# Performance work log

Measured on AMD Instinct MI355X. Metric: run time of the kernel, lower is better.

The kernel has to match this reference:

```python
import jax, jax.numpy as jnp
import numpy as np

N = 96                       # max_num_nodes == input_dim
LATENT = 256
OUT_DIM = N * (N + 1) // 2   # 4656
MPM_ITERS = 50


def setup_inputs() -> dict:
    key = jax.random.key(0)
    ks = jax.random.split(key, 8)
    s = 0.05
    return {
        "input_features": jax.random.normal(ks[0], (1, N, N), jnp.float32),
        "adj": jax.random.uniform(ks[1], (1, N, N), jnp.float32),
        "eps": jax.random.normal(ks[2], (1, LATENT), jnp.float32),
        "We11": jax.random.normal(ks[3], (N * N, LATENT), jnp.float32) * s,
        "be11": jnp.zeros((LATENT,), jnp.float32),
        "We12": jax.random.normal(ks[4], (N * N, LATENT), jnp.float32) * s,
        "be12": jnp.zeros((LATENT,), jnp.float32),
        "Wd1": jax.random.normal(ks[5], (LATENT, LATENT), jnp.float32) * s,
        "bd1": jnp.zeros((LATENT,), jnp.float32),
        "Wd2": jax.random.normal(ks[6], (LATENT, OUT_DIM), jnp.float32) * s,
        "bd2": jnp.zeros((OUT_DIM,), jnp.float32),
    }


def _bce(inp, tgt):
    # torch F.binary_cross_entropy(input=inp, target=tgt) with log clamp -100
    li = jnp.clip(jnp.log(inp), -100.0)
    l1 = jnp.clip(jnp.log1p(-inp), -100.0)
    return -jnp.mean(tgt * li + (1.0 - tgt) * l1)


def reference(input_features, adj, eps, We11, be11, We12, be12, Wd1, bd1, Wd2, bd2):
    # ---- MLP_VAE_plain ----
    h = input_features.reshape(-1, N * N)              # [1, N*N]
    z_mu = h @ We11 + be11
    z_ls = h @ We12 + be12
    z = eps * jnp.exp(0.5 * z_ls) + z_mu
    y = jax.nn.relu(z @ Wd1 + bd1) @ Wd2 + bd2         # [1, OUT_DIM]
    out = jax.nn.sigmoid(y)

    # ---- recover recon adjacency from triu vector (detached in original) ----
    iu, ju = jnp.triu_indices(N)
    up = jnp.zeros((N, N), jnp.float32).at[iu, ju].set(out[0])
    adj_rec = up + up.T - jnp.diag(jnp.diag(up))

    adj0 = adj[0]
    feat = jnp.sum(adj0, axis=1)                       # degree features
    feat_r = jnp.sum(adj_rec, axis=1)

    # ---- edge similarity tensor S[i,j,a,b] (vectorized O(N^4)) ----
    d = jnp.diag(adj0)
    dr = jnp.diag(adj_rec)
    A = adj0 * d[:, None] * d[None, :]                 # adj[i,j]*adj[i,i]*adj[j,j]
    B = adj_rec * dr[:, None] * dr[None, :]
    off = 1.0 - jnp.eye(N, dtype=jnp.float32)
    S = (A * off)[:, :, None, None] * (B * off)[None, None, :, :]  # i!=j, a!=b
    sim = 1.0 / (jnp.abs(feat[:, None] - feat_r[None, :]) + 1.0)   # deg_feature_similarity
    Sd = d[:, None] * dr[None, :] * sim                # S[i,i,a,a]
    r = jnp.arange(N)
    S = S.at[r[:, None], r[:, None], r[None, :], r[None, :]].set(Sd)

    # ---- max-pool matching (mpm), 50 iterations ----
    x0 = jnp.full((N, N), 1.0 / N, jnp.float32)

    def step(x, _):
        pooled = jnp.max(S * x[None, :, None, :], axis=3)          # [i,j,a]
        x_new = x * Sd + jnp.einsum('ija,ij->ia', pooled, off)     # sum over j != i
        return x_new / jnp.linalg.norm(x_new), None

    assignment, _ = jax.lax.scan(step, x0, None, length=MPM_ITERS)
    # (original then calls scipy Hungarian and only prints; result is unused in loss)

    # ---- loss ----
    adj_vec = adj0[iu, ju]                             # detached in original
    recon_loss = _bce(adj_vec, out[0])
    kl = -0.5 * jnp.sum(1.0 + z_ls - z_mu ** 2 - jnp.exp(z_ls)) / (N * N)
    loss = recon_loss + kl
    return loss, assignment
```

## Files before the change

### kernel.cpp

```cpp
#include <hip/hip_runtime.h>
#include <math.h>

typedef unsigned long long ull;

#define N      96
#define NN     9216
#define LAT    256
#define ODIM   4656
#define CH     128
#define RPC    72
#define ITERS  50
#define CB     12
#define CT     768
#define CPB    8

#define SGNMASK2 0x8000000080000000ULL
#define ABSMASK2 0x7FFFFFFF7FFFFFFFULL

#define WS_PART  0
#define WS_OUTS  65536
#define WS_KL    70192
#define WS_BCE   70193
#define WS_NSLOT 70208
#define WS_XBUF  70592

__device__ __forceinline__ int tri(int i, int j) {
    return i * N - i * (i - 1) / 2 + (j - i);
}

__device__ __forceinline__ int tri_row(int o) {
    int i = (int)floorf((193.0f - sqrtf((float)(37249 - 8 * o))) * 0.5f);
    i = max(0, min(95, i));
    while ((i + 1) * N - (i + 1) * i / 2 <= o) ++i;
    while (i * N - i * (i - 1) / 2 > o) --i;
    return i;
}

__global__ __launch_bounds__(256) void kA_gemv(const float* __restrict__ h,
                                               const float* __restrict__ W1,
                                               const float* __restrict__ W2,
                                               float* __restrict__ ws) {
    __shared__ float hs[RPC];
    int t = threadIdx.x, c = blockIdx.x;
    if (c == 0) {
        if (t < 2) ws[WS_KL + t] = 0.f;
        if (t < CB * 16) {
            ws[WS_NSLOT + t]           = 0.0f;
            ws[WS_NSLOT + CB * 16 + t] = -0.0f;
        }
    }
    for (int z = c * 256 + t; z < NN; z += CH * 256) {
        ws[WS_XBUF + z]      = 0.0f;
        ws[WS_XBUF + NN + z] = -0.0f;
    }
    int k0 = c * RPC;
    if (t < RPC) hs[t] = h[k0 + t];
    __syncthreads();
    float a1 = 0.f, a2 = 0.f;
    #pragma unroll 4
    for (int kk = 0; kk < RPC; ++kk) {
        float hv = hs[kk];
        a1 = fmaf(hv, W1[(k0 + kk) * LAT + t], a1);
        a2 = fmaf(hv, W2[(k0 + kk) * LAT + t], a2);
    }
    ws[WS_PART + c * LAT + t]        = a1;
    ws[WS_PART + (CH + c) * LAT + t] = a2;
}

__global__ __launch_bounds__(256) void kB_dec(const float* __restrict__ eps,
                                              const float* __restrict__ be11,
                                              const float* __restrict__ be12,
                                              const float* __restrict__ Wd1,
                                              const float* __restrict__ bd1,
                                              const float* __restrict__ Wd2,
                                              const float* __restrict__ bd2,
                                              const float* __restrict__ adj,
                                              float* __restrict__ ws) {
    __shared__ float zi[LAT];
    __shared__ float hid[LAT];
    __shared__ float red[256];
    int t = threadIdx.x;
    const float* p = ws + WS_PART;
    float mu = 0.f, ls = 0.f;
    #pragma unroll 8
    for (int c = 0; c < CH; ++c) {
        mu += p[c * LAT + t];
        ls += p[(CH + c) * LAT + t];
    }
    mu += be11[t];
    ls += be12[t];
    zi[t] = eps[t] * expf(0.5f * ls) + mu;
    red[t] = 1.0f + ls - mu * mu - expf(ls);
    __syncthreads();
    for (int s = 128; s > 0; s >>= 1) {
        if (t < s) red[t] += red[t + s];
        __syncthreads();
    }
    if (blockIdx.x == 0 && t == 0) ws[WS_KL] = -0.5f * red[0] / 9216.0f;
    __syncthreads();
    float acc = 0.f;
    #pragma unroll 8
    for (int k = 0; k < LAT; ++k) acc = fmaf(zi[k], Wd1[k * LAT + t], acc);
    hid[t] = fmaxf(acc + bd1[t], 0.f);
    __syncthreads();
    int o = blockIdx.x * 256 + t;
    float term = 0.f;
    if (o < ODIM) {
        float a2 = 0.f;
        #pragma unroll 8
        for (int k = 0; k < LAT; ++k) a2 = fmaf(hid[k], Wd2[k * ODIM + o], a2);
        float y = a2 + bd2[o];
        float s = 1.0f / (1.0f + expf(-y));
        ws[WS_OUTS + o] = s;
        int i = tri_row(o);
        int j = i + (o - (i * N - i * (i - 1) / 2));
        float inp = adj[i * N + j];
        float li = fmaxf(logf(inp), -100.0f);
        float l1 = fmaxf(log1pf(-inp), -100.0f);
        term = s * li + (1.0f - s) * l1;
    }
    red[t] = term;
    __syncthreads();
    for (int s = 128; s > 0; s >>= 1) {
        if (t < s) red[t] += red[t + s];
        __syncthreads();
    }
    if (t == 0) atomicAdd(ws + WS_BCE, red[0]);
}

__global__ __launch_bounds__(CT, 3) void kC_mpm(const float* __restrict__ adj,
                                                float* __restrict__ ws,
                                                float* __restrict__ out) {
    __shared__ float xnT[N][97];
    __shared__ float Brow[CPB][N];
    __shared__ float Scol[CPB][N];
    __shared__ float Mv[CPB][N];
    __shared__ float ds[N], drs[N], ft[N];
    __shared__ float ftr_sh[CPB];
    __shared__ float wred[CT / 64];
    __shared__ float s_inv;

    int t = threadIdx.x, bid = blockIdx.x;
    int jj = t % N, al = t / N;
    int a  = bid * CPB + al;

    const float* outs = ws + WS_OUTS;
    float* xbuf  = ws + WS_XBUF;
    float* nslot = ws + WS_NSLOT;

    if (t < N) {
        ds[t]  = adj[t * N + t];
        drs[t] = outs[tri(t, t)];
        const float4* ar = (const float4*)(adj + t * N);
        float s1 = 0.f;
        #pragma unroll
        for (int q = 0; q < N / 4; ++q) {
            float4 v = ar[q];
            s1 += v.x + v.y + v.z + v.w;
        }
        ft[t] = s1;
    }
    __syncthreads();
    {
        int lo = min(a, jj), hi = max(a, jj);
        Mv[al][jj] = outs[tri(lo, hi)];
    }
    __syncthreads();
    if (t < CPB) {
        float s2 = 0.f;
        for (int b = 0; b < N; ++b) s2 += Mv[t][b];
        ftr_sh[t] = s2;
    }
    __syncthreads();
    Brow[al][jj] = (jj == a) ? 0.f : (Mv[al][jj] * drs[a]) * drs[jj];
    Scol[al][jj] = (ds[jj] * drs[a]) * (1.0f / (fabsf(ft[jj] - ftr_sh[al]) + 1.0f));

    float arow[N];
    {
        const float* arp = adj + jj * N;
        float di = ds[jj];
        #pragma unroll
        for (int j = 0; j < N; ++j)
            arow[j] = (j == jj) ? 0.f : (arp[j] * di) * ds[j];
    }
    __syncthreads();

    float acc = 0.f;
    for (int s = 0; s < ITERS; ++s) {
        if (s == 0) {
            const float v0 = (float)(1.0 / 96.0);
            for (int f = t; f < NN; f += CT) xnT[f / N][f % N] = v0;
            if (t == 0) s_inv = 1.0f;
        } else {
            const ull want = ((s >> 1) & 1) ? SGNMASK2 : 0ULL;
            const ull* src = (const ull*)(xbuf + (s & 1) * NN);
            ull v[6];
            bool ok = false;
            while (!ok) {
                ok = true;
                #pragma unroll
                for (int k = 0; k < 6; ++k)
                    v[k] = __hip_atomic_load(&src[k * CT + t], __ATOMIC_RELAXED,
                                             __HIP_MEMORY_SCOPE_AGENT);
                #pragma unroll
                for (int k = 0; k < 6; ++k)
                    ok &= ((v[k] & SGNMASK2) == want);
                if (!ok) __builtin_amdgcn_s_sleep(1);
            }
            #pragma unroll
            for (int k = 0; k < 6; ++k) {
                ull w = v[k] & ABSMASK2;
                int e = (k * CT + t) * 2;
                int ac = e / N, i = e % N;
                xnT[ac][i]     = __uint_as_float((unsigned)w);
                xnT[ac][i + 1] = __uint_as_float((unsigned)(w >> 32));
            }
            if (t < 64) {
                const unsigned esn = (unsigned)((s >> 1) & 1);
                float pv = 0.f;
                bool done = (t >= CB);
                const unsigned* np = (const unsigned*)(nslot + (s & 1) * CB * 16);
                while (!__all(done)) {
                    if (!done) {
                        unsigned u = __hip_atomic_load(&np[t * 16], __ATOMIC_RELAXED,
                                                       __HIP_MEMORY_SCOPE_AGENT);
                        if ((u >> 31) == esn) { pv = __uint_as_float(u & 0x7FFFFFFFu); done = true; }
                    }
                    __builtin_amdgcn_s_sleep(1);
                }
                #pragma unroll
                for (int off = 8; off > 0; off >>= 1) pv += __shfl_xor(pv, off, 16);
                if (t == 0) s_inv = 1.0f / sqrtf(pv);
            }
        }
        __syncthreads();

        float m = 0.f;
        #pragma unroll
        for (int bq = 0; bq < N / 4; ++bq) {
            m = fmaxf(m, Brow[al][bq * 4 + 0] * xnT[bq * 4 + 0][jj]);
            m = fmaxf(m, Brow[al][bq * 4 + 1] * xnT[bq * 4 + 1][jj]);
            m = fmaxf(m, Brow[al][bq * 4 + 2] * xnT[bq * 4 + 2][jj]);
            m = fmaxf(m, Brow[al][bq * 4 + 3] * xnT[bq * 4 + 3][jj]);
        }
        Mv[al][jj] = m;
        __syncthreads();

        float r = xnT[a][jj] * Scol[al][jj];
        #pragma unroll
        for (int q = 0; q < N / 4; ++q) {
            float4 mv = *(const float4*)&Mv[al][q * 4];
            r = fmaf(arow[q * 4 + 0], mv.x, r);
            r = fmaf(arow[q * 4 + 1], mv.y, r);
            r = fmaf(arow[q * 4 + 2], mv.z, r);
            r = fmaf(arow[q * 4 + 3], mv.w, r);
        }
        acc = r * s_inv;

        const unsigned tag1 = (unsigned)(((s + 1) >> 1) & 1);
        float nx = __shfl_down(acc, 1);
        if (s < ITERS - 1 && (t & 1) == 0) {
            ull pv = (ull)__float_as_uint(acc) | ((ull)__float_as_uint(nx) << 32);
            if (tag1) pv |= SGNMASK2;
            __hip_atomic_store((ull*)(xbuf + ((s + 1) & 1) * NN) + ((a * N + jj) >> 1),
                               pv, __ATOMIC_RELAXED, __HIP_MEMORY_SCOPE_AGENT);
        }

        float ssq = acc * acc;
        #pragma unroll
        for (int off = 32; off > 0; off >>= 1) ssq += __shfl_xor(ssq, off);
        if ((t & 63) == 0) wred[t >> 6] = ssq;
        __syncthreads();
        if (t == 0) {
            float sum = 0.f;
            #pragma unroll
            for (int w = 0; w < CT / 64; ++w) sum += wred[w];
            unsigned u = __float_as_uint(sum) | (tag1 << 31);
            __hip_atomic_store((unsigned*)(nslot + ((s + 1) & 1) * CB * 16 + bid * 16),
                               u, __ATOMIC_RELAXED, __HIP_MEMORY_SCOPE_AGENT);
        }
    }

    if (t < 64) {
        const unsigned esf = (unsigned)((ITERS >> 1) & 1);
        float pv = 0.f;
        bool done = (t >= CB);
        const unsigned* np = (const unsigned*)(nslot + (ITERS & 1) * CB * 16);
        while (!__all(done)) {
            if (!done) {
                unsigned u = __hip_atomic_load(&np[t * 16], __ATOMIC_RELAXED,
                                               __HIP_MEMORY_SCOPE_AGENT);
                if ((u >> 31) == esf) { pv = __uint_as_float(u & 0x7FFFFFFFu); done = true; }
            }
            __builtin_amdgcn_s_sleep(1);
        }
        #pragma unroll
        for (int off = 8; off > 0; off >>= 1) pv += __shfl_xor(pv, off, 16);
        if (t == 0) s_inv = 1.0f / sqrtf(pv);
    }
    __syncthreads();
    out[1 + jj * N + a] = acc * s_inv;
    if (bid == 0 && t == 0)
        out[0] = -(ws[WS_BCE] / 4656.0f) + ws[WS_KL];
}

extern "C" void kernel_launch(void* const* d_in, const int* in_sizes, int n_in,
                              void* d_out, int out_size, void* d_ws, size_t ws_size,
                              hipStream_t stream) {
    const float* inf  = (const float*)d_in[0];
    const float* adj  = (const float*)d_in[1];
    const float* eps  = (const float*)d_in[2];
    const float* We11 = (const float*)d_in[3];
    const float* be11 = (const float*)d_in[4];
    const float* We12 = (const float*)d_in[5];
    const float* be12 = (const float*)d_in[6];
    const float* Wd1  = (const float*)d_in[7];
    const float* bd1  = (const float*)d_in[8];
    const float* Wd2  = (const float*)d_in[9];
    const float* bd2  = (const float*)d_in[10];
    float* ws  = (float*)d_ws;
    float* out = (float*)d_out;

    kA_gemv<<<CH, 256, 0, stream>>>(inf, We11, We12, ws);
    kB_dec <<<19, 256, 0, stream>>>(eps, be11, be12, Wd1, bd1, Wd2, bd2, adj, ws);
    kC_mpm <<<CB, CT, 0, stream>>>(adj, ws, out);
}
```

Measured before the change: 365.9 us.

## Compute norm locally from gathered x instead of cross-block norm slots

Drops the separate per-block sum-of-squares slots and the polling on them. Each block now recomputes the global norm from the full x vector it already gathers every iteration, reducing it across its waves in shared memory. This removes one inter-block handshake and a block barrier per iteration. In exchange, every block does redundant squared-sum work, and the final iteration must also publish and re-gather the whole x vector to normalise the output.

```diff
diff --git a/kernel.cpp b/kernel.cpp
--- a/kernel.cpp
+++ b/kernel.cpp
@@ -21,7 +21,6 @@
 #define WS_OUTS  65536
 #define WS_KL    70192
 #define WS_BCE   70193
-#define WS_NSLOT 70208
 #define WS_XBUF  70592
 
 __device__ __forceinline__ int tri(int i, int j) {
@@ -42,13 +41,7 @@
                                                float* __restrict__ ws) {
     __shared__ float hs[RPC];
     int t = threadIdx.x, c = blockIdx.x;
-    if (c == 0) {
-        if (t < 2) ws[WS_KL + t] = 0.f;
-        if (t < CB * 16) {
-            ws[WS_NSLOT + t]           = 0.0f;
-            ws[WS_NSLOT + CB * 16 + t] = -0.0f;
-        }
-    }
+    if (c == 0 && t < 2) ws[WS_KL + t] = 0.f;
     for (int z = c * 256 + t; z < NN; z += CH * 256) {
         ws[WS_XBUF + z]      = 0.0f;
         ws[WS_XBUF + NN + z] = -0.0f;
@@ -138,15 +131,14 @@
     __shared__ float ds[N], drs[N], ft[N];
     __shared__ float ftr_sh[CPB];
     __shared__ float wred[CT / 64];
-    __shared__ float s_inv;
 
     int t = threadIdx.x, bid = blockIdx.x;
+    int wv = t >> 6;
     int jj = t % N, al = t / N;
     int a  = bid * CPB + al;
 
     const float* outs = ws + WS_OUTS;
     float* xbuf  = ws + WS_XBUF;
-    float* nslot = ws + WS_NSLOT;
 
     if (t < N) {
         ds[t]  = adj[t * N + t];
@@ -190,7 +182,6 @@
         if (s == 0) {
             const float v0 = (float)(1.0 / 96.0);
             for (int f = t; f < NN; f += CT) xnT[f / N][f % N] = v0;
-            if (t == 0) s_inv = 1.0f;
         } else {
             const ull want = ((s >> 1) & 1) ? SGNMASK2 : 0ULL;
             const ull* src = (const ull*)(xbuf + (s & 1) * NN);
@@ -207,31 +198,21 @@
                     ok &= ((v[k] & SGNMASK2) == want);
                 if (!ok) __builtin_amdgcn_s_sleep(1);
             }
+            float tssq = 0.f;
             #pragma unroll
             for (int k = 0; k < 6; ++k) {
                 ull w = v[k] & ABSMASK2;
                 int e = (k * CT + t) * 2;
                 int ac = e / N, i = e % N;
-                xnT[ac][i]     = __uint_as_float((unsigned)w);
-                xnT[ac][i + 1] = __uint_as_float((unsigned)(w >> 32));
+                float f0 = __uint_as_float((unsigned)w);
+                float f1 = __uint_as_float((unsigned)(w >> 32));
+                xnT[ac][i]     = f0;
+                xnT[ac][i + 1] = f1;
+                tssq = fmaf(f0, f0, fmaf(f1, f1, tssq));
             }
-            if (t < 64) {
-                const unsigned esn = (unsigned)((s >> 1) & 1);
-                float pv = 0.f;
-                bool done = (t >= CB);
-                const unsigned* np = (const unsigned*)(nslot + (s & 1) * CB * 16);
-                while (!__all(done)) {
-                    if (!done) {
-                        unsigned u = __hip_atomic_load(&np[t * 16], __ATOMIC_RELAXED,
-                                                       __HIP_MEMORY_SCOPE_AGENT);
-                        if ((u >> 31) == esn) { pv = __uint_as_float(u & 0x7FFFFFFFu); done = true; }
-                    }
-                    __builtin_amdgcn_s_sleep(1);
-                }
-                #pragma unroll
-                for (int off = 8; off > 0; off >>= 1) pv += __shfl_xor(pv, off, 16);
-                if (t == 0) s_inv = 1.0f / sqrtf(pv);
-            }
+            #pragma unroll
+            for (int off = 32; off > 0; off >>= 1) tssq += __shfl_xor(tssq, off);
+            if ((t & 63) == 0) wred[wv] = tssq;
         }
         __syncthreads();
 
@@ -245,6 +226,16 @@
         }
         Mv[al][jj] = m;
         __syncthreads();
+
+        float s_inv;
+        if (s == 0) {
+            s_inv = 1.0f;
+        } else {
+            float sum = 0.f;
+            #pragma unroll
+            for (int w = 0; w < CT / 64; ++w) sum += wred[w];
+            s_inv = 1.0f / sqrtf(sum);
+        }
 
         float r = xnT[a][jj] * Scol[al][jj];
         #pragma unroll
@@ -259,49 +250,51 @@
 
         const unsigned tag1 = (unsigned)(((s + 1) >> 1) & 1);
         float nx = __shfl_down(acc, 1);
-        if (s < ITERS - 1 && (t & 1) == 0) {
+        if ((t & 1) == 0) {
             ull pv = (ull)__float_as_uint(acc) | ((ull)__float_as_uint(nx) << 32);
             if (tag1) pv |= SGNMASK2;
             __hip_atomic_store((ull*)(xbuf + ((s + 1) & 1) * NN) + ((a * N + jj) >> 1),
                                pv, __ATOMIC_RELAXED, __HIP_MEMORY_SCOPE_AGENT);
         }
-
-        float ssq = acc * acc;
-        #pragma unroll
-        for (int off = 32; off > 0; off >>= 1) ssq += __shfl_xor(ssq, off);
-        if ((t & 63) == 0) wred[t >> 6] = ssq;
-        __syncthreads();
-        if (t == 0) {
-            float sum = 0.f;
-            #pragma unroll
-            for (int w = 0; w < CT / 64; ++w) sum += wred[w];
-            unsigned u = __float_as_uint(sum) | (tag1 << 31);
-            __hip_atomic_store((unsigned*)(nslot + ((s + 1) & 1) * CB * 16 + bid * 16),
-                               u, __ATOMIC_RELAXED, __HIP_MEMORY_SCOPE_AGENT);
-        }
-    }
-
-    if (t < 64) {
-        const unsigned esf = (unsigned)((ITERS >> 1) & 1);
-        float pv = 0.f;
-        bool done = (t >= CB);
-        const unsigned* np = (const unsigned*)(nslot + (ITERS & 1) * CB * 16);
-        while (!__all(done)) {
-            if (!done) {
-                unsigned u = __hip_atomic_load(&np[t * 16], __ATOMIC_RELAXED,
-                                               __HIP_MEMORY_SCOPE_AGENT);
-                if ((u >> 31) == esf) { pv = __uint_as_float(u & 0x7FFFFFFFu); done = true; }
-            }
-            __builtin_amdgcn_s_sleep(1);
-        }
-        #pragma unroll
-        for (int off = 8; off > 0; off >>= 1) pv += __shfl_xor(pv, off, 16);
-        if (t == 0) s_inv = 1.0f / sqrtf(pv);
-    }
-    __syncthreads();
-    out[1 + jj * N + a] = acc * s_inv;
-    if (bid == 0 && t == 0)
-        out[0] = -(ws[WS_BCE] / 4656.0f) + ws[WS_KL];
+        __syncthreads();
+    }
+
+    {
+        const ull want = ((ITERS >> 1) & 1) ? SGNMASK2 : 0ULL;
+        const ull* src = (const ull*)(xbuf + (ITERS & 1) * NN);
+        ull v[6];
+        bool ok = false;
+        while (!ok) {
+            ok = true;
+            #pragma unroll
+            for (int k = 0; k < 6; ++k)
+                v[k] = __hip_atomic_load(&src[k * CT + t], __ATOMIC_RELAXED,
+                                         __HIP_MEMORY_SCOPE_AGENT);
+            #pragma unroll
+            for (int k = 0; k < 6; ++k)
+                ok &= ((v[k] & SGNMASK2) == want);
+            if (!ok) __builtin_amdgcn_s_sleep(1);
+        }
+        float tssq = 0.f;
+        #pragma unroll
+        for (int k = 0; k < 6; ++k) {
+            ull w = v[k] & ABSMASK2;
+            float f0 = __uint_as_float((unsigned)w);
+            float f1 = __uint_as_float((unsigned)(w >> 32));
+            tssq = fmaf(f0, f0, fmaf(f1, f1, tssq));
+        }
+        #pragma unroll
+        for (int off = 32; off > 0; off >>= 1) tssq += __shfl_xor(tssq, off);
+        if ((t & 63) == 0) wred[wv] = tssq;
+        __syncthreads();
+        float sum = 0.f;
+        #pragma unroll
+        for (int w = 0; w < CT / 64; ++w) sum += wred[w];
+        float s_invf = 1.0f / sqrtf(sum);
+        out[1 + jj * N + a] = acc * s_invf;
+        if (bid == 0 && t == 0)
+            out[0] = -(ws[WS_BCE] / 4656.0f) + ws[WS_KL];
+    }
 }
 
 extern "C" void kernel_launch(void* const* d_in, const int* in_sizes, int n_in,
```

Result: no change. 364.2 us (-0.5%).
